# Kernel tuning notes

Hardware: AMD Instinct MI355X
Metric: run time of the kernel (lower is better)

## Reference

```python
import jax, jax.numpy as jnp
import numpy as np

NUM_EXPERTS = 64
Z_LOSS_COEF = 0.001
AUX_LOSS_COEF = 0.001
GROUPS, TOKENS = 64, 8192


def setup_inputs() -> dict:
    key = jax.random.key(0)
    k1, = jax.random.split(key, 1)
    router_logits = jax.random.normal(k1, (GROUPS, TOKENS, NUM_EXPERTS), dtype=jnp.float32)
    attention_mask = jnp.ones((GROUPS, TOKENS), dtype=jnp.int32)  # unused by forward, kept for fidelity
    return {"router_logits": router_logits, "attention_mask": attention_mask, "expert_capacity": 160}


def reference(router_logits, attention_mask, expert_capacity):
    g, t, e = router_logits.shape

    # --- router z-loss: mean over (groups, tokens) of logsumexp^2 ---
    log_z = jax.nn.logsumexp(router_logits, axis=-1)            # [g, t]
    z_loss = jnp.sum(log_z * log_z) / (g * t)

    # --- softmax probs ---
    router_probs = jax.nn.softmax(router_logits, axis=-1)       # [g, t, e]

    # --- recompute expert indices with capacity masking ---
    expert_index = jnp.argmax(router_probs, axis=-1)            # [g, t]
    oh = jax.nn.one_hot(expert_index, e, dtype=jnp.int32)       # [g, t, e]
    token_priority = jnp.cumsum(oh, axis=-2)                    # running count per expert
    capacity_mask = token_priority <= expert_capacity
    oh_masked = oh * capacity_mask.astype(jnp.int32)
    # if token dropped (row all zero), argmax -> 0, matching torch semantics
    expert_index = jnp.argmax(oh_masked, axis=-1)               # [g, t]

    # --- load-balancing aux loss ---
    expert_mask = jax.nn.one_hot(expert_index, e, dtype=jnp.float32)  # [g, t, e]
    tokens_per_group_and_expert = jnp.mean(expert_mask, axis=-2)       # [g, e]
    router_prob_per_group_and_expert = jnp.mean(router_probs, axis=-2) # [g, e]
    aux_loss = jnp.mean(tokens_per_group_and_expert * router_prob_per_group_and_expert) * (e ** 2)

    return Z_LOSS_COEF * z_loss + AUX_LOSS_COEF * aux_loss
```

## Files before the change

kernel.cpp:

```cpp
#include <hip/hip_runtime.h>

#define NG 64
#define NT 8192
#define NE 64
#define Z_COEF 0.001f
#define A_COEF 0.001f

#define BLK 512
#define ITERS 4
#define TPW 64
#define TPB 512
#define NBLK (NG * (NT / TPB))

#define DPP_XOR1  0xB1
#define DPP_XOR2  0x4E
#define DPP_HMIRR 0x141
#define DPP_MIRR  0x140

template <int CTRL>
__device__ __forceinline__ float fdpp(float x) {
    return __int_as_float(__builtin_amdgcn_mov_dpp(__float_as_int(x), CTRL, 0xF, 0xF, true));
}
template <int CTRL>
__device__ __forceinline__ int idpp(int x) {
    return __builtin_amdgcn_mov_dpp(x, CTRL, 0xF, 0xF, true);
}

template <int CTRL>
__device__ __forceinline__ void bfly_maxidx(float& m, int& me) {
    const float om  = fdpp<CTRL>(m);
    const int   ome = idpp<CTRL>(me);
    const bool  u   = (om > m) || (om == m && ome < me);
    me = u ? ome : me;
    m  = fmaxf(m, om);
}


__global__ __launch_bounds__(BLK) void router_main(
    const float* __restrict__ logits,
    float* __restrict__ probsum,
    unsigned int* __restrict__ cnt,
    float* __restrict__ zsum)
{
    const int tid  = threadIdx.x;
    const int lane = tid & 63;
    const int wv   = tid >> 6;
    const int c    = lane & 15;

    const int g     = blockIdx.x >> 4;
    const int tbase = (blockIdx.x & 15) * TPB + wv * TPW;

    const float* p0 = logits + ((size_t)g * NT + tbase) * NE + lane * 4;

    __shared__ float        s_ps[NE];
    __shared__ unsigned int s_cnt[NE];
    __shared__ float        s_z;
    if (tid < NE) { s_ps[tid] = 0.f; s_cnt[tid] = 0u; }
    if (tid == 0) s_z = 0.f;
    __syncthreads();

    float accp[4] = {0.f, 0.f, 0.f, 0.f};
    float accz = 0.f;

    float4 cur[4], nxt[4];
#pragma unroll
    for (int k = 0; k < 4; ++k)
        cur[k] = *reinterpret_cast<const float4*>(p0 + k * 256);

    for (int it = 0; it < ITERS; ++it) {
        const int nit = (it + 1 < ITERS) ? (it + 1) : it;
        const float* pn = p0 + (size_t)nit * 1024;
#pragma unroll
        for (int k = 0; k < 4; ++k)
            nxt[k] = *reinterpret_cast<const float4*>(pn + k * 256);

#pragma unroll
        for (int k = 0; k < 4; ++k) {
            const float v0 = cur[k].x, v1 = cur[k].y, v2 = cur[k].z, v3 = cur[k].w;

            float m = v0; int mi = 0;
            if (v1 > m) { m = v1; mi = 1; }
            if (v2 > m) { m = v2; mi = 2; }
            if (v3 > m) { m = v3; mi = 3; }
            int me = (c << 2) + mi;
            const float ml = m;

            const float e0 = __expf(v0 - ml), e1 = __expf(v1 - ml);
            const float e2 = __expf(v2 - ml), e3 = __expf(v3 - ml);
            float s = (e0 + e1) + (e2 + e3);

            bfly_maxidx<DPP_XOR1>(m, me);
            bfly_maxidx<DPP_XOR2>(m, me);
            bfly_maxidx<DPP_HMIRR>(m, me);
            bfly_maxidx<DPP_MIRR>(m, me);

            const float r = __expf(ml - m);
            s *= r;
            s += fdpp<DPP_XOR1>(s);
            s += fdpp<DPP_XOR2>(s);
            s += fdpp<DPP_HMIRR>(s);
            s += fdpp<DPP_MIRR>(s);

            const float wsc = r * __builtin_amdgcn_rcpf(s);
            accp[0] += e0 * wsc;
            accp[1] += e1 * wsc;
            accp[2] += e2 * wsc;
            accp[3] += e3 * wsc;

            if (c == 0) {
                const float lz = m + __logf(s);
                accz += lz * lz;
                atomicAdd(&s_cnt[me], 1u);
            }
        }
#pragma unroll
        for (int k = 0; k < 4; ++k) cur[k] = nxt[k];
    }

#pragma unroll
    for (int j = 0; j < 4; ++j) {
        accp[j] += __shfl_xor(accp[j], 16);
        accp[j] += __shfl_xor(accp[j], 32);
    }
    if (lane < 16) {
#pragma unroll
        for (int j = 0; j < 4; ++j) atomicAdd(&s_ps[(c << 2) + j], accp[j]);
    }
    if (c == 0) atomicAdd(&s_z, accz);
    __syncthreads();

    if (tid < NE) {
        atomicAdd(&probsum[g * NE + tid], s_ps[tid]);
        atomicAdd(&cnt[g * NE + tid], s_cnt[tid]);
    }
    if (tid == 0) atomicAdd(&zsum[g], s_z);
}

__global__ __launch_bounds__(1024) void router_final(
    const float* __restrict__ probsum,
    const unsigned int* __restrict__ cnt,
    const float* __restrict__ zsum,
    const int* __restrict__ capp,
    float* __restrict__ out)
{
    const int tid  = threadIdx.x;
    const int lane = tid & 63;
    const int w    = tid >> 6;
    const unsigned int C = (unsigned int)(*capp);

    __shared__ float s_aux[16];
    __shared__ float s_zz;

    float acc = 0.f;
    for (int g = w; g < NG; g += 16) {
        const unsigned int n = cnt[g * NE + lane];
        const float        P = probsum[g * NE + lane];

        float ovf = (n > C) ? (float)(n - C) : 0.f;
#pragma unroll
        for (int off = 1; off <= 32; off <<= 1) ovf += __shfl_xor(ovf, off);

        float ce = fminf((float)n, (float)C);
        if (lane == 0) ce += ovf;
        acc += ce * P;
    }
#pragma unroll
    for (int off = 1; off <= 32; off <<= 1) acc += __shfl_xor(acc, off);
    if (lane == 0) s_aux[w] = acc;

    if (w == 0) {
        float zz = zsum[lane];
#pragma unroll
        for (int off = 1; off <= 32; off <<= 1) zz += __shfl_xor(zz, off);
        if (lane == 0) s_zz = zz;
    }
    __syncthreads();

    if (tid == 0) {
        float A = 0.f;
#pragma unroll
        for (int i = 0; i < 16; ++i) A += s_aux[i];
        const float aux_loss = A * ((float)NE / ((float)NG * (float)NT * (float)NT));
        const float z_loss   = s_zz / ((float)NG * (float)NT);
        out[0] = Z_COEF * z_loss + A_COEF * aux_loss;
    }
}

extern "C" void kernel_launch(void* const* d_in, const int* in_sizes, int n_in,
                              void* d_out, int out_size, void* d_ws, size_t ws_size,
                              hipStream_t stream)
{
    const float* logits = (const float*)d_in[0];
    const int* cap = (const int*)d_in[2];

    float*        probsum = (float*)d_ws;
    unsigned int* cntp    = (unsigned int*)((char*)d_ws + (size_t)NG * NE * 4);
    float*        zsum    = (float*)((char*)d_ws + 2ull * NG * NE * 4);

    hipMemsetAsync(d_ws, 0, 2ull * NG * NE * 4 + NG * 4, stream);

    router_main<<<NBLK, BLK, 0, stream>>>(logits, probsum, cntp, zsum);
    router_final<<<1, 1024, 0, stream>>>(probsum, cntp, zsum, cap, (float*)d_out);
}
```

Before: 40.03 us.

## Write per-block partials instead of global atomics and drop workspace memset

Each main-kernel block now writes its per-expert probability sums, counts and z partial to its own workspace row instead of atomically accumulating into per-group slots. The final kernel sums the 16 block rows per group and all 1024 z partials itself. This removes global atomic contention and the separate memset launch. In exchange the single-block final kernel reads a larger workspace (about 512 KB) serially.

After: 37.12 us. 1.08x faster.

```diff
diff --git a/kernel.cpp b/kernel.cpp
--- a/kernel.cpp
+++ b/kernel.cpp
@@ -38,9 +38,9 @@
 
 __global__ __launch_bounds__(BLK) void router_main(
     const float* __restrict__ logits,
-    float* __restrict__ probsum,
-    unsigned int* __restrict__ cnt,
-    float* __restrict__ zsum)
+    float* __restrict__ pps,
+    unsigned int* __restrict__ pcnt,
+    float* __restrict__ pz)
 {
     const int tid  = threadIdx.x;
     const int lane = tid & 63;
@@ -129,17 +129,18 @@
     if (c == 0) atomicAdd(&s_z, accz);
     __syncthreads();
 
+    const int row = blockIdx.x;
     if (tid < NE) {
-        atomicAdd(&probsum[g * NE + tid], s_ps[tid]);
-        atomicAdd(&cnt[g * NE + tid], s_cnt[tid]);
-    }
-    if (tid == 0) atomicAdd(&zsum[g], s_z);
+        pps [row * NE + tid] = s_ps[tid];
+        pcnt[row * NE + tid] = s_cnt[tid];
+    }
+    if (tid == 0) pz[row] = s_z;
 }
 
 __global__ __launch_bounds__(1024) void router_final(
-    const float* __restrict__ probsum,
-    const unsigned int* __restrict__ cnt,
-    const float* __restrict__ zsum,
+    const float* __restrict__ pps,
+    const unsigned int* __restrict__ pcnt,
+    const float* __restrict__ pz,
     const int* __restrict__ capp,
     float* __restrict__ out)
 {
@@ -149,17 +150,23 @@
     const unsigned int C = (unsigned int)(*capp);
 
     __shared__ float s_aux[16];
-    __shared__ float s_zz;
+    __shared__ float s_zz[16];
 
     float acc = 0.f;
-    for (int g = w; g < NG; g += 16) {
-        const unsigned int n = cnt[g * NE + lane];
-        const float        P = probsum[g * NE + lane];
-
+#pragma unroll
+    for (int gi = 0; gi < NG / 16; ++gi) {
+        const int g = w + gi * 16;
+        unsigned int n = 0u;
+        float        P = 0.f;
+#pragma unroll
+        for (int b = 0; b < 16; ++b) {
+            const int row = g * 16 + b;
+            n += pcnt[row * NE + lane];
+            P += pps [row * NE + lane];
+        }
         float ovf = (n > C) ? (float)(n - C) : 0.f;
 #pragma unroll
         for (int off = 1; off <= 32; off <<= 1) ovf += __shfl_xor(ovf, off);
-
         float ce = fminf((float)n, (float)C);
         if (lane == 0) ce += ovf;
         acc += ce * P;
@@ -168,20 +175,18 @@
     for (int off = 1; off <= 32; off <<= 1) acc += __shfl_xor(acc, off);
     if (lane == 0) s_aux[w] = acc;
 
-    if (w == 0) {
-        float zz = zsum[lane];
-#pragma unroll
-        for (int off = 1; off <= 32; off <<= 1) zz += __shfl_xor(zz, off);
-        if (lane == 0) s_zz = zz;
-    }
+    float zz = pz[tid];
+#pragma unroll
+    for (int off = 1; off <= 32; off <<= 1) zz += __shfl_xor(zz, off);
+    if (lane == 0) s_zz[w] = zz;
     __syncthreads();
 
     if (tid == 0) {
-        float A = 0.f;
-#pragma unroll
-        for (int i = 0; i < 16; ++i) A += s_aux[i];
+        float A = 0.f, Z = 0.f;
+#pragma unroll
+        for (int i = 0; i < 16; ++i) { A += s_aux[i]; Z += s_zz[i]; }
         const float aux_loss = A * ((float)NE / ((float)NG * (float)NT * (float)NT));
-        const float z_loss   = s_zz / ((float)NG * (float)NT);
+        const float z_loss   = Z / ((float)NG * (float)NT);
         out[0] = Z_COEF * z_loss + A_COEF * aux_loss;
     }
 }
@@ -193,12 +198,10 @@
     const float* logits = (const float*)d_in[0];
     const int* cap = (const int*)d_in[2];
 
-    float*        probsum = (float*)d_ws;
-    unsigned int* cntp    = (unsigned int*)((char*)d_ws + (size_t)NG * NE * 4);
-    float*        zsum    = (float*)((char*)d_ws + 2ull * NG * NE * 4);
-
-    hipMemsetAsync(d_ws, 0, 2ull * NG * NE * 4 + NG * 4, stream);
-
-    router_main<<<NBLK, BLK, 0, stream>>>(logits, probsum, cntp, zsum);
-    router_final<<<1, 1024, 0, stream>>>(probsum, cntp, zsum, cap, (float*)d_out);
-}
+    float*        pps  = (float*)d_ws;
+    unsigned int* pcnt = (unsigned int*)((char*)d_ws + (size_t)NBLK * NE * 4);
+    float*        pz   = (float*)((char*)d_ws + 2ull * NBLK * NE * 4);
+
+    router_main<<<NBLK, BLK, 0, stream>>>(logits, pps, pcnt, pz);
+    router_final<<<1, 1024, 0, stream>>>(pps, pcnt, pz, cap, (float*)d_out);
+}
```
